# Kernel optimization log

Measured on AMD Instinct MI355X. Metric: run time of the kernel, lower is better.

The kernel has to match this reference:

```python
import jax, jax.numpy as jnp
import numpy as np

N_NODES = 100000
N_EDGES = 1600000
D = 128
N_GRAPHS = 1024
N_LAYERS = 3
BN_EPS = 1e-5


def setup_inputs() -> dict:
    key = jax.random.key(0)
    ks = jax.random.split(key, 12)
    x = jax.random.normal(ks[0], (N_NODES, D), dtype=jnp.float32)
    edge_index = jax.random.randint(ks[1], (2, N_EDGES), 0, N_NODES, dtype=jnp.int32)
    batch = jnp.sort(jax.random.randint(ks[2], (N_NODES,), 0, N_GRAPHS, dtype=jnp.int32))
    scale = 1.0 / np.sqrt(D)
    W1 = jax.random.uniform(ks[3], (D, D), jnp.float32, -scale, scale)
    b1 = jax.random.uniform(ks[4], (D,), jnp.float32, -scale, scale)
    W2 = jax.random.uniform(ks[5], (D, D), jnp.float32, -scale, scale)
    b2 = jax.random.uniform(ks[6], (D,), jnp.float32, -scale, scale)
    W3 = jax.random.uniform(ks[7], (D, D), jnp.float32, -scale, scale)
    b3 = jax.random.uniform(ks[8], (D,), jnp.float32, -scale, scale)
    eps = jnp.zeros((N_LAYERS,), jnp.float32)          # GINConv train_eps init = 0
    gamma = jnp.ones((N_LAYERS, D), jnp.float32)       # BatchNorm1d weight
    beta = jnp.zeros((N_LAYERS, D), jnp.float32)       # BatchNorm1d bias
    return {"x": x, "edge_index": edge_index, "batch": batch,
            "W1": W1, "b1": b1, "W2": W2, "b2": b2, "W3": W3, "b3": b3,
            "eps": eps, "gamma": gamma, "beta": beta}


def _gin_layer(h, src, dst, W, b, eps_i, g, bt):
    # scatter-add neighbor aggregation: sum_{j in N(i)} h_j
    agg = jax.ops.segment_sum(h[src], dst, num_segments=N_NODES)  # [N, D]
    h = (1.0 + eps_i) * h + agg
    h = h @ W.T + b                                   # Linear
    mean = jnp.mean(h, axis=0)                        # BatchNorm1d (training, biased var)
    var = jnp.var(h, axis=0)
    h = (h - mean) * jax.lax.rsqrt(var + BN_EPS) * g + bt
    return jax.nn.relu(h)


def reference(x, edge_index, batch, W1, b1, W2, b2, W3, b3, eps, gamma, beta):
    src, dst = edge_index[0], edge_index[1]
    h = x
    for i, (W, b) in enumerate([(W1, b1), (W2, b2), (W3, b3)]):
        h = _gin_layer(h, src, dst, W, b, eps[i], gamma[i], beta[i])
    # global mean pool over graphs
    sums = jax.ops.segment_sum(h, batch, num_segments=N_GRAPHS)             # [G, D]
    counts = jax.ops.segment_sum(jnp.ones((h.shape[0],), h.dtype), batch,
                                 num_segments=N_GRAPHS)                      # [G]
    return sums / jnp.maximum(counts, 1.0)[:, None]
```

## Files before the change

kernel.cpp:

```cpp
#include <hip/hip_runtime.h>

#define N_NODES 100000
#define N_PAD 100032
#define N_EDGES 1600000
#define DIM 128
#define N_GRAPHS 1024

#define SCAN_BLOCK 256
#define SCAN_NB ((N_NODES + SCAN_BLOCK - 1) / SCAN_BLOCK)

#define NPART 8
#define PART_SZ 12500

typedef __bf16 bf16x8 __attribute__((ext_vector_type(8)));
typedef float f32x4 __attribute__((ext_vector_type(4)));

__device__ __forceinline__ unsigned short f2bf(float f) {
    unsigned u = __builtin_bit_cast(unsigned, f);
    u += 0x7fffu + ((u >> 16) & 1u);
    return (unsigned short)(u >> 16);
}
__device__ __forceinline__ unsigned pk2(float a, float b) {
    return (unsigned)f2bf(a) | ((unsigned)f2bf(b) << 16);
}
__device__ __forceinline__ float bf2f(unsigned short s) {
    return __builtin_bit_cast(float, (unsigned)s << 16);
}
__device__ __forceinline__ void dec2(unsigned p, float& lo, float& hi) {
    lo = __builtin_bit_cast(float, p << 16);
    hi = __builtin_bit_cast(float, p & 0xffff0000u);
}

template <bool BN>
__device__ __forceinline__ void acc8(uint4 p, float* a, const float* sc, const float* sh) {
    float v[8];
    dec2(p.x, v[0], v[1]);
    dec2(p.y, v[2], v[3]);
    dec2(p.z, v[4], v[5]);
    dec2(p.w, v[6], v[7]);
#pragma unroll
    for (int j = 0; j < 8; ++j) {
        float t = BN ? fmaxf(fmaf(v[j], sc[j], sh[j]), 0.f) : v[j];
        a[j] += t;
    }
}


__global__ __launch_bounds__(256) void hist_kernel(const int* __restrict__ dst,
                                                   int* __restrict__ deg) {
    int i = blockIdx.x * blockDim.x + threadIdx.x;
    int stride = gridDim.x * blockDim.x;
    const int NE4 = N_EDGES / 4;
    for (; i < NE4; i += stride) {
        int4 d4 = ((const int4*)dst)[i];
        atomicAdd(&deg[d4.x], 1);
        atomicAdd(&deg[d4.y], 1);
        atomicAdd(&deg[d4.z], 1);
        atomicAdd(&deg[d4.w], 1);
    }
}

__global__ __launch_bounds__(256) void fill_part_kernel(const int* __restrict__ src,
                                                        const int* __restrict__ dst,
                                                        int* __restrict__ cursor,
                                                        int* __restrict__ csr) {
    int p = blockIdx.x & (NPART - 1);
    int bgrp = blockIdx.x >> 3;
    int nb = gridDim.x >> 3;
    int tid = bgrp * blockDim.x + threadIdx.x;
    int nthreads = nb * blockDim.x;
    const int NE8 = N_EDGES / 8;
    for (int i = tid; i < NE8; i += nthreads) {
        int4 da = ((const int4*)dst)[2 * i];
        int4 db = ((const int4*)dst)[2 * i + 1];
        int4 sa = ((const int4*)src)[2 * i];
        int4 sb = ((const int4*)src)[2 * i + 1];
        if (da.x / PART_SZ == p) csr[atomicAdd(&cursor[da.x], 1)] = sa.x;
        if (da.y / PART_SZ == p) csr[atomicAdd(&cursor[da.y], 1)] = sa.y;
        if (da.z / PART_SZ == p) csr[atomicAdd(&cursor[da.z], 1)] = sa.z;
        if (da.w / PART_SZ == p) csr[atomicAdd(&cursor[da.w], 1)] = sa.w;
        if (db.x / PART_SZ == p) csr[atomicAdd(&cursor[db.x], 1)] = sb.x;
        if (db.y / PART_SZ == p) csr[atomicAdd(&cursor[db.y], 1)] = sb.y;
        if (db.z / PART_SZ == p) csr[atomicAdd(&cursor[db.z], 1)] = sb.z;
        if (db.w / PART_SZ == p) csr[atomicAdd(&cursor[db.w], 1)] = sb.w;
    }
}


__global__ __launch_bounds__(SCAN_BLOCK) void scan_partial_kernel(const int* __restrict__ deg,
                                                                  int* __restrict__ partials) {
    __shared__ int red[SCAN_BLOCK / 64];
    int i = blockIdx.x * SCAN_BLOCK + threadIdx.x;
    int v = (i < N_NODES) ? deg[i] : 0;
    for (int o = 32; o > 0; o >>= 1) v += __shfl_down(v, o, 64);
    if ((threadIdx.x & 63) == 0) red[threadIdx.x >> 6] = v;
    __syncthreads();
    if (threadIdx.x == 0) {
        int s = 0;
#pragma unroll
        for (int w = 0; w < SCAN_BLOCK / 64; ++w) s += red[w];
        partials[blockIdx.x] = s;
    }
}

__global__ __launch_bounds__(512) void scan_partials_kernel(int* __restrict__ partials,
                                                            int* __restrict__ off) {
    __shared__ int sm[512];
    int t = threadIdx.x;
    int v = (t < SCAN_NB) ? partials[t] : 0;
    sm[t] = v;
    __syncthreads();
    for (int o = 1; o < 512; o <<= 1) {
        int u = (t >= o) ? sm[t - o] : 0;
        __syncthreads();
        sm[t] += u;
        __syncthreads();
    }
    if (t < SCAN_NB) partials[t] = sm[t] - v;
    if (t == 0) off[N_NODES] = sm[511];
}

__global__ __launch_bounds__(SCAN_BLOCK) void scan_scatter_kernel(const int* __restrict__ deg,
                                                                  const int* __restrict__ partials,
                                                                  int* __restrict__ off,
                                                                  int* __restrict__ cursor) {
    __shared__ int sm[SCAN_BLOCK];
    int t = threadIdx.x;
    int i = blockIdx.x * SCAN_BLOCK + t;
    int v = (i < N_NODES) ? deg[i] : 0;
    sm[t] = v;
    __syncthreads();
    for (int o = 1; o < SCAN_BLOCK; o <<= 1) {
        int u = (t >= o) ? sm[t - o] : 0;
        __syncthreads();
        sm[t] += u;
        __syncthreads();
    }
    if (i < N_NODES) {
        int r = partials[blockIdx.x] + sm[t] - v;
        off[i] = r;
        cursor[i] = r;
    }
}


__global__ __launch_bounds__(64) void wprep_kernel(const float* __restrict__ W1,
                                                   const float* __restrict__ W2,
                                                   const float* __restrict__ W3,
                                                   uint4* __restrict__ wb4) {
    int b = blockIdx.x;
    int l = b >> 5;
    int nt = (b >> 2) & 7;
    int kk = b & 3;
    int lane = threadIdx.x;
    const float* W = (l == 0) ? W1 : (l == 1) ? W2 : W3;
    int row = nt * 16 + (lane & 15);
    int cb = kk * 32 + (lane >> 4) * 8;
    const float* g = W + row * DIM + cb;
    float4 f0 = *(const float4*)g;
    float4 f1 = *(const float4*)(g + 4);
    uint4 o;
    o.x = pk2(f0.x, f0.y);
    o.y = pk2(f0.z, f0.w);
    o.z = pk2(f1.x, f1.y);
    o.w = pk2(f1.z, f1.w);
    wb4[(size_t)b * 64 + lane] = o;
}


__global__ __launch_bounds__(256) void xconv_kernel(const float* __restrict__ x,
                                                    unsigned short* __restrict__ xb) {
    int i = blockIdx.x * blockDim.x + threadIdx.x;
    int stride = gridDim.x * blockDim.x;
    const int TOT = N_PAD * DIM / 8;
    for (; i < TOT; i += stride) {
        int row = i >> 4;
        int ks = i & 15;
        uint4 o = {0, 0, 0, 0};
        if (row < N_NODES) {
            const float* g = x + (size_t)row * DIM + ks * 8;
            float4 f0 = *(const float4*)g;
            float4 f1 = *(const float4*)(g + 4);
            o.x = pk2(f0.x, f0.y);
            o.y = pk2(f0.z, f0.w);
            o.z = pk2(f1.x, f1.y);
            o.w = pk2(f1.z, f1.w);
        }
        ((uint4*)xb)[i] = o;
    }
}


template <bool BN>
__global__ __launch_bounds__(256) void agg_gemm_kernel(const unsigned short* __restrict__ hin,
                                                       const int* __restrict__ off,
                                                       const int* __restrict__ csr,
                                                       const float* __restrict__ eps_arr, int layer,
                                                       const float* __restrict__ csum_prev,
                                                       const float* __restrict__ csq_prev,
                                                       const float* __restrict__ gamma_prev,
                                                       const float* __restrict__ beta_prev,
                                                       const uint4* __restrict__ wb4,
                                                       unsigned short* __restrict__ y,
                                                       float* __restrict__ csum_out,
                                                       float* __restrict__ csq_out) {
    __shared__ unsigned short tile[64 * DIM];
    __shared__ float sstat[4][DIM];
    __shared__ float sstatq[4][DIM];
    int tid = threadIdx.x;
    int row0 = blockIdx.x * 64;
    int wv = tid >> 6;
    int esl = (tid >> 4) & 3;
    int dl = tid & 15;
    float se = 1.0f + eps_arr[layer];
    float sc[8], sh[8];
    if (BN) {
#pragma unroll
        for (int j = 0; j < 8; ++j) {
            int d = dl * 8 + j;
            float m = csum_prev[d] * (1.0f / N_NODES);
            float var = csq_prev[d] * (1.0f / N_NODES) - m * m;
            float s = gamma_prev[d] * rsqrtf(var + 1e-5f);
            sc[j] = s;
            sh[j] = beta_prev[d] - m * s;
        }
    }
    const uint4* base = (const uint4*)hin + dl;
    const size_t RS = DIM / 8;

#pragma unroll 1
    for (int r = 0; r < 16; ++r) {
        int trow = wv * 16 + r;
        int row = row0 + trow;
        float a[8] = {0.f, 0.f, 0.f, 0.f, 0.f, 0.f, 0.f, 0.f};
        float s8[8] = {0.f, 0.f, 0.f, 0.f, 0.f, 0.f, 0.f, 0.f};
        if (row < N_NODES) {
            {
                uint4 pv = base[(size_t)row * RS];
                float v[8];
                dec2(pv.x, v[0], v[1]); dec2(pv.y, v[2], v[3]);
                dec2(pv.z, v[4], v[5]); dec2(pv.w, v[6], v[7]);
#pragma unroll
                for (int j = 0; j < 8; ++j)
                    s8[j] = BN ? fmaxf(fmaf(v[j], sc[j], sh[j]), 0.f) : v[j];
            }
            int k = off[row], e = off[row + 1];
            for (; k + 8 <= e; k += 8) {
                int i0 = csr[k + esl];
                int i1 = csr[k + 4 + esl];
                uint4 p0 = base[(size_t)i0 * RS];
                uint4 p1 = base[(size_t)i1 * RS];
                acc8<BN>(p0, a, sc, sh);
                acc8<BN>(p1, a, sc, sh);
            }
            for (; k < e; k += 4) {
                int kk = k + esl;
                if (kk < e) {
                    uint4 p0 = base[(size_t)csr[kk] * RS];
                    acc8<BN>(p0, a, sc, sh);
                }
            }
        }
#pragma unroll
        for (int j = 0; j < 8; ++j) {
            a[j] += __shfl_xor(a[j], 16);
            a[j] += __shfl_xor(a[j], 32);
            a[j] = fmaf(se, s8[j], a[j]);
        }
        if (esl == 0) {
            uint4 pw;
            pw.x = pk2(a[0], a[1]);
            pw.y = pk2(a[2], a[3]);
            pw.z = pk2(a[4], a[5]);
            pw.w = pk2(a[6], a[7]);
            int byte = (trow * 256 + dl * 16) ^ ((trow & 7) << 4);
            *(uint4*)((char*)tile + byte) = pw;
        }
    }
    __syncthreads();

    int w = tid >> 6;
    int l = tid & 63;
    int lr = l & 15;
    int lg = l >> 4;
    bf16x8 a[4];
#pragma unroll
    for (int kk = 0; kk < 4; ++kk) {
        int row = w * 16 + lr;
        int byte = (row * 256 + kk * 64 + lg * 16) ^ ((row & 7) << 4);
        a[kk] = __builtin_bit_cast(bf16x8, *(uint4*)((char*)tile + byte));
    }

#pragma unroll
    for (int nt = 0; nt < 8; ++nt) {
        f32x4 acc = {0.0f, 0.0f, 0.0f, 0.0f};
#pragma unroll
        for (int kk = 0; kk < 4; ++kk) {
            bf16x8 b = __builtin_bit_cast(bf16x8, wb4[(nt * 4 + kk) * 64 + l]);
            acc = __builtin_amdgcn_mfma_f32_16x16x32_bf16(a[kk], b, acc, 0, 0, 0);
        }
        int col = nt * 16 + lr;
        size_t base2 = (size_t)(row0 + w * 16 + lg * 4) * DIM + col;
        y[base2] = f2bf(acc[0]);
        y[base2 + DIM] = f2bf(acc[1]);
        y[base2 + 2 * DIM] = f2bf(acc[2]);
        y[base2 + 3 * DIM] = f2bf(acc[3]);
        float s = acc[0] + acc[1] + acc[2] + acc[3];
        float q = acc[0] * acc[0] + acc[1] * acc[1] + acc[2] * acc[2] + acc[3] * acc[3];
        s += __shfl_xor(s, 16);
        s += __shfl_xor(s, 32);
        q += __shfl_xor(q, 16);
        q += __shfl_xor(q, 32);
        if (lg == 0) {
            sstat[w][col] = s;
            sstatq[w][col] = q;
        }
    }
    __syncthreads();
    if (tid < DIM) {
        float s = sstat[0][tid] + sstat[1][tid] + sstat[2][tid] + sstat[3][tid];
        float q = sstatq[0][tid] + sstatq[1][tid] + sstatq[2][tid] + sstatq[3][tid];
        atomicAdd(&csum_out[tid], s);
        atomicAdd(&csq_out[tid], q);
    }
}


__global__ __launch_bounds__(128) void pool_kernel(const unsigned short* __restrict__ y,
                                                   const int* __restrict__ batch,
                                                   const float* __restrict__ csum,
                                                   const float* __restrict__ csq,
                                                   const float* __restrict__ gamma,
                                                   const float* __restrict__ beta,
                                                   float* __restrict__ out) {
    int gph = blockIdx.x;
    int d = threadIdx.x;
    float m = csum[d] * (1.0f / N_NODES);
    float var = csq[d] * (1.0f / N_NODES) - m * m;
    float sc = gamma[d] * rsqrtf(var + 1e-5f);
    float sh = beta[d] - m * sc;
    int lo = 0, hi = N_NODES;
    while (lo < hi) {
        int mid = (lo + hi) >> 1;
        if (batch[mid] < gph) lo = mid + 1; else hi = mid;
    }
    int start = lo;
    hi = N_NODES;
    while (lo < hi) {
        int mid = (lo + hi) >> 1;
        if (batch[mid] < gph + 1) lo = mid + 1; else hi = mid;
    }
    int end = lo;
    float s0 = 0.f, s1 = 0.f, s2 = 0.f, s3 = 0.f;
    int n = start;
    for (; n + 3 < end; n += 4) {
        float v0 = bf2f(y[(size_t)n * DIM + d]);
        float v1 = bf2f(y[(size_t)(n + 1) * DIM + d]);
        float v2 = bf2f(y[(size_t)(n + 2) * DIM + d]);
        float v3 = bf2f(y[(size_t)(n + 3) * DIM + d]);
        s0 += fmaxf(fmaf(v0, sc, sh), 0.0f);
        s1 += fmaxf(fmaf(v1, sc, sh), 0.0f);
        s2 += fmaxf(fmaf(v2, sc, sh), 0.0f);
        s3 += fmaxf(fmaf(v3, sc, sh), 0.0f);
    }
    for (; n < end; ++n) {
        float v = bf2f(y[(size_t)n * DIM + d]);
        s0 += fmaxf(fmaf(v, sc, sh), 0.0f);
    }
    float s = (s0 + s1) + (s2 + s3);
    out[gph * DIM + d] = s / fmaxf((float)(end - start), 1.0f);
}


extern "C" void kernel_launch(void* const* d_in, const int* in_sizes, int n_in,
                              void* d_out, int out_size, void* d_ws, size_t ws_size,
                              hipStream_t stream) {
    const float* x = (const float*)d_in[0];
    const int* ei = (const int*)d_in[1];
    const int* batch = (const int*)d_in[2];
    const float* Wp[3] = {(const float*)d_in[3], (const float*)d_in[5], (const float*)d_in[7]};
    const float* eps = (const float*)d_in[9];
    const float* gamma = (const float*)d_in[10];
    const float* beta = (const float*)d_in[11];
    float* out = (float*)d_out;

    char* ws = (char*)d_ws;
    size_t o = 0;
    auto alloc = [&](size_t bytes) {
        void* p = ws + o;
        o = (o + bytes + 255) & ~(size_t)255;
        return p;
    };
    int* deg = (int*)alloc(N_NODES * sizeof(int));
    int* off = (int*)alloc((N_NODES + 1) * sizeof(int));
    int* cursor = (int*)alloc(N_NODES * sizeof(int));
    int* partials = (int*)alloc(SCAN_NB * sizeof(int));
    int* csr = (int*)alloc(N_EDGES * sizeof(int));
    uint4* wb4 = (uint4*)alloc(3 * 8 * 4 * 64 * 16);
    float* csums = (float*)alloc(3 * DIM * sizeof(float));
    float* csqs = (float*)alloc(3 * DIM * sizeof(float));
    unsigned short* xb = (unsigned short*)alloc((size_t)N_PAD * DIM * 2);
    unsigned short* y0 = (unsigned short*)alloc((size_t)N_PAD * DIM * 2);
    unsigned short* y1 = (unsigned short*)alloc((size_t)N_PAD * DIM * 2);

    hipMemsetAsync(deg, 0, N_NODES * sizeof(int), stream);
    hipMemsetAsync(csums, 0, 3 * DIM * sizeof(float), stream);
    hipMemsetAsync(csqs, 0, 3 * DIM * sizeof(float), stream);

    hist_kernel<<<1024, 256, 0, stream>>>(ei + N_EDGES, deg);
    scan_partial_kernel<<<SCAN_NB, SCAN_BLOCK, 0, stream>>>(deg, partials);
    scan_partials_kernel<<<1, 512, 0, stream>>>(partials, off);
    scan_scatter_kernel<<<SCAN_NB, SCAN_BLOCK, 0, stream>>>(deg, partials, off, cursor);
    fill_part_kernel<<<2048, 256, 0, stream>>>(ei, ei + N_EDGES, cursor, csr);
    wprep_kernel<<<96, 64, 0, stream>>>(Wp[0], Wp[1], Wp[2], wb4);
    xconv_kernel<<<2048, 256, 0, stream>>>(x, xb);

    const int NBLK = N_PAD / 64;
    agg_gemm_kernel<false><<<NBLK, 256, 0, stream>>>(xb, off, csr, eps, 0,
                                                     nullptr, nullptr, nullptr, nullptr,
                                                     wb4, y0, csums, csqs);
    agg_gemm_kernel<true><<<NBLK, 256, 0, stream>>>(y0, off, csr, eps, 1,
                                                    csums, csqs, gamma, beta,
                                                    wb4 + 2048, y1, csums + DIM, csqs + DIM);
    agg_gemm_kernel<true><<<NBLK, 256, 0, stream>>>(y1, off, csr, eps, 2,
                                                    csums + DIM, csqs + DIM, gamma + DIM, beta + DIM,
                                                    wb4 + 4096, y0, csums + 2 * DIM, csqs + 2 * DIM);
    pool_kernel<<<N_GRAPHS, DIM, 0, stream>>>(y0, batch, csums + 2 * DIM, csqs + 2 * DIM,
                                              gamma + 2 * DIM, beta + 2 * DIM, out);
}
```

Measured before the change: 581.5 us.

## Halve agg-gemm tile rows, split MFMA columns across waves, deepen gather unroll

The fused aggregation+GEMM kernel now handles 32 rows per block instead of 64, doubling the grid. The four waves split the MFMA work as two row tiles by two column groups, and the column statistics are reduced accordingly. The neighbour gather loop gets a 16-edge unrolled stage so more row loads are in flight. The CSR fill also uses 4 destination partitions instead of 8. The aim is more blocks and more memory-level parallelism for the latency-bound gather, at the cost of twice as many per-block stat atomics.

```diff
diff --git a/kernel.cpp b/kernel.cpp
--- a/kernel.cpp
+++ b/kernel.cpp
@@ -9,8 +9,10 @@
 #define SCAN_BLOCK 256
 #define SCAN_NB ((N_NODES + SCAN_BLOCK - 1) / SCAN_BLOCK)
 
-#define NPART 8
-#define PART_SZ 12500
+#define NPART 4
+#define PART_SZ 25000
+
+#define TROWS 32
 
 typedef __bf16 bf16x8 __attribute__((ext_vector_type(8)));
 typedef float f32x4 __attribute__((ext_vector_type(4)));
@@ -65,8 +67,8 @@
                                                         int* __restrict__ cursor,
                                                         int* __restrict__ csr) {
     int p = blockIdx.x & (NPART - 1);
-    int bgrp = blockIdx.x >> 3;
-    int nb = gridDim.x >> 3;
+    int bgrp = blockIdx.x >> 2;
+    int nb = gridDim.x >> 2;
     int tid = bgrp * blockDim.x + threadIdx.x;
     int nthreads = nb * blockDim.x;
     const int NE8 = N_EDGES / 8;
@@ -204,11 +206,11 @@
                                                        unsigned short* __restrict__ y,
                                                        float* __restrict__ csum_out,
                                                        float* __restrict__ csq_out) {
-    __shared__ unsigned short tile[64 * DIM];
-    __shared__ float sstat[4][DIM];
-    __shared__ float sstatq[4][DIM];
+    __shared__ unsigned short tile[TROWS * DIM];
+    __shared__ float sstat[4][64];
+    __shared__ float sstatq[4][64];
     int tid = threadIdx.x;
-    int row0 = blockIdx.x * 64;
+    int row0 = blockIdx.x * TROWS;
     int wv = tid >> 6;
     int esl = (tid >> 4) & 3;
     int dl = tid & 15;
@@ -229,8 +231,8 @@
     const size_t RS = DIM / 8;
 
 #pragma unroll 1
-    for (int r = 0; r < 16; ++r) {
-        int trow = wv * 16 + r;
+    for (int r = 0; r < 8; ++r) {
+        int trow = wv * 8 + r;
         int row = row0 + trow;
         float a[8] = {0.f, 0.f, 0.f, 0.f, 0.f, 0.f, 0.f, 0.f};
         float s8[8] = {0.f, 0.f, 0.f, 0.f, 0.f, 0.f, 0.f, 0.f};
@@ -245,6 +247,20 @@
                     s8[j] = BN ? fmaxf(fmaf(v[j], sc[j], sh[j]), 0.f) : v[j];
             }
             int k = off[row], e = off[row + 1];
+            for (; k + 16 <= e; k += 16) {
+                int i0 = csr[k + esl];
+                int i1 = csr[k + 4 + esl];
+                int i2 = csr[k + 8 + esl];
+                int i3 = csr[k + 12 + esl];
+                uint4 p0 = base[(size_t)i0 * RS];
+                uint4 p1 = base[(size_t)i1 * RS];
+                uint4 p2 = base[(size_t)i2 * RS];
+                uint4 p3 = base[(size_t)i3 * RS];
+                acc8<BN>(p0, a, sc, sh);
+                acc8<BN>(p1, a, sc, sh);
+                acc8<BN>(p2, a, sc, sh);
+                acc8<BN>(p3, a, sc, sh);
+            }
             for (; k + 8 <= e; k += 8) {
                 int i0 = csr[k + esl];
                 int i1 = csr[k + 4 + esl];
@@ -283,16 +299,19 @@
     int l = tid & 63;
     int lr = l & 15;
     int lg = l >> 4;
+    int rt = w & 1;
+    int cg = w >> 1;
     bf16x8 a[4];
 #pragma unroll
     for (int kk = 0; kk < 4; ++kk) {
-        int row = w * 16 + lr;
+        int row = rt * 16 + lr;
         int byte = (row * 256 + kk * 64 + lg * 16) ^ ((row & 7) << 4);
         a[kk] = __builtin_bit_cast(bf16x8, *(uint4*)((char*)tile + byte));
     }
 
 #pragma unroll
-    for (int nt = 0; nt < 8; ++nt) {
+    for (int ntl = 0; ntl < 4; ++ntl) {
+        int nt = cg * 4 + ntl;
         f32x4 acc = {0.0f, 0.0f, 0.0f, 0.0f};
 #pragma unroll
         for (int kk = 0; kk < 4; ++kk) {
@@ -300,7 +319,7 @@
             acc = __builtin_amdgcn_mfma_f32_16x16x32_bf16(a[kk], b, acc, 0, 0, 0);
         }
         int col = nt * 16 + lr;
-        size_t base2 = (size_t)(row0 + w * 16 + lg * 4) * DIM + col;
+        size_t base2 = (size_t)(row0 + rt * 16 + lg * 4) * DIM + col;
         y[base2] = f2bf(acc[0]);
         y[base2 + DIM] = f2bf(acc[1]);
         y[base2 + 2 * DIM] = f2bf(acc[2]);
@@ -312,14 +331,16 @@
         q += __shfl_xor(q, 16);
         q += __shfl_xor(q, 32);
         if (lg == 0) {
-            sstat[w][col] = s;
-            sstatq[w][col] = q;
+            sstat[w][col & 63] = s;
+            sstatq[w][col & 63] = q;
         }
     }
     __syncthreads();
     if (tid < DIM) {
-        float s = sstat[0][tid] + sstat[1][tid] + sstat[2][tid] + sstat[3][tid];
-        float q = sstatq[0][tid] + sstatq[1][tid] + sstatq[2][tid] + sstatq[3][tid];
+        int cg2 = tid >> 6;
+        int c = tid & 63;
+        float s = sstat[cg2 * 2][c] + sstat[cg2 * 2 + 1][c];
+        float q = sstatq[cg2 * 2][c] + sstatq[cg2 * 2 + 1][c];
         atomicAdd(&csum_out[tid], s);
         atomicAdd(&csq_out[tid], q);
     }
@@ -415,7 +436,7 @@
     wprep_kernel<<<96, 64, 0, stream>>>(Wp[0], Wp[1], Wp[2], wb4);
     xconv_kernel<<<2048, 256, 0, stream>>>(x, xb);
 
-    const int NBLK = N_PAD / 64;
+    const int NBLK = N_PAD / TROWS;
     agg_gemm_kernel<false><<<NBLK, 256, 0, stream>>>(xb, off, csr, eps, 0,
                                                      nullptr, nullptr, nullptr, nullptr,
                                                      wb4, y0, csums, csqs);
```

Result: slower. 651.2 us (+12.0%).
